# Performance work log

Measured on AMD Instinct MI355X. Metric: run time of the kernel, lower is better.

The kernel has to match this reference:

```python
import jax, jax.numpy as jnp
import numpy as np

# NF4 codebook (from bitsandbytes/torchao)
NF4 = jnp.array([
    -1.0, -0.6961928009986877, -0.5250730514526367, -0.39491748809814453,
    -0.28444138169288635, -0.18477343022823334, -0.09105003625154495, 0.0,
    0.07958029955625534, 0.16093020141124725, 0.24611230194568634,
    0.33791524171829224, 0.44070982933044434, 0.5626170039176941,
    0.7229568362236023, 1.0], dtype=jnp.float32)

IN_DIM, OUT_DIM = 4096, 4096
RANK, ALPHA = 16, 32.0
BLOCK = 64            # nf4 quantization block size
SCALER_BLOCK = 256    # double-quantization block size for scalers


def setup_inputs() -> dict:
    key = jax.random.key(0)
    kx, kw, ka, kb = jax.random.split(key, 4)
    x = jax.random.normal(kx, (4, 2048, IN_DIM), jnp.float32)
    # float base weight, then quantize to NF4 with double-quantized scalers
    w = jax.random.normal(kw, (OUT_DIM, IN_DIM), jnp.float32) * 0.02
    blocks = w.reshape(-1, BLOCK)                          # [n_blocks, 64]
    scalers = jnp.max(jnp.abs(blocks), axis=1)             # per-block absmax
    scaler_mean = jnp.mean(scalers, keepdims=True)         # [1]
    sc = (scalers - scaler_mean).reshape(-1, SCALER_BLOCK) # [n_sblocks, 256]
    q_factor = 127.0 / jnp.max(jnp.abs(sc), axis=1)        # [n_sblocks]
    q_scalers = jnp.clip(jnp.round(sc * q_factor[:, None]), -127, 127)
    q_scalers = q_scalers.astype(jnp.int32).reshape(-1)    # [n_blocks]
    # map normalized values to nearest NF4 code via bucket midpoints
    norm = blocks / scalers[:, None]
    mid = (NF4[:-1] + NF4[1:]) * 0.5
    nf4_idx = jnp.searchsorted(mid, norm).astype(jnp.int32)  # [n_blocks, 64]
    # LoRA weights (kaiming-uniform-like)
    lora_a_w = jax.random.uniform(ka, (RANK, IN_DIM), jnp.float32, -1.0, 1.0) / jnp.sqrt(IN_DIM)
    lora_b_w = jax.random.uniform(kb, (OUT_DIM, RANK), jnp.float32, -1.0, 1.0) / jnp.sqrt(RANK)
    return dict(x=x, nf4_idx=nf4_idx, q_scalers=q_scalers, q_factor=q_factor,
                scaler_mean=scaler_mean, lora_a_w=lora_a_w, lora_b_w=lora_b_w)


def _dequant_nf4(nf4_idx, q_scalers, q_factor, scaler_mean):
    # dequantize double-quantized scalers, then blocks
    scalers = q_scalers.astype(jnp.float32) / jnp.repeat(q_factor, SCALER_BLOCK) + scaler_mean[0]
    w = NF4[nf4_idx] * scalers[:, None]                    # [n_blocks, 64]
    return w.reshape(OUT_DIM, IN_DIM)


def reference(x, nf4_idx, q_scalers, q_factor, scaler_mean, lora_a_w, lora_b_w):
    w = _dequant_nf4(nf4_idx, q_scalers, q_factor, scaler_mean)  # [out, in]
    base = jnp.einsum('bsd,od->bso', x, w)
    # dropout p=0.0 -> identity
    lora = jnp.einsum('bsr,or->bso', jnp.einsum('bsd,rd->bsr', x, lora_a_w), lora_b_w)
    return base + (ALPHA / RANK) * lora
```

## Files before the change

### kernel.cpp

```cpp
#include <hip/hip_runtime.h>
#include <hip/hip_bf16.h>

typedef unsigned short u16;
typedef u16 u16x4 __attribute__((ext_vector_type(4)));
typedef __bf16 bf16x8 __attribute__((ext_vector_type(8)));
typedef float f32x4 __attribute__((ext_vector_type(4)));

#define IN_DIM 4096
#define OUT_DIM 4096
#define M_TOT 8192

__device__ __constant__ float NF4_LUT[16] = {
    -1.0f, -0.6961928009986877f, -0.5250730514526367f, -0.39491748809814453f,
    -0.28444138169288635f, -0.18477343022823334f, -0.09105003625154495f, 0.0f,
    0.07958029955625534f, 0.16093020141124725f, 0.24611230194568634f,
    0.33791524171829224f, 0.44070982933044434f, 0.5626170039176941f,
    0.7229568362236023f, 1.0f};

__device__ __forceinline__ u16 f2bf(float f) {
  unsigned i = __float_as_uint(f);
  i += 0x7fffu + ((i >> 16) & 1u);
  return (u16)(i >> 16);
}

__global__ __launch_bounds__(256) void convert_x(
    const float4* __restrict__ xin, u16x4* __restrict__ xout, int n4)
{
  int i = blockIdx.x * 256 + threadIdx.x;
  const int stride = gridDim.x * 256;
  for (; i < n4; i += stride) {
    const float4 v = xin[i];
    u16x4 o;
    o.x = f2bf(v.x); o.y = f2bf(v.y); o.z = f2bf(v.z); o.w = f2bf(v.w);
    xout[i] = o;
  }
}

__global__ __launch_bounds__(256) void dequant_fold(
    const int* __restrict__ nf4_idx, const int* __restrict__ q_scalers,
    const float* __restrict__ q_factor, const float* __restrict__ scaler_mean,
    const float* __restrict__ lora_a, const float* __restrict__ lora_b,
    u16* __restrict__ w_eff)
{
  __shared__ float s_lut[16];
  __shared__ float s_b[16];
  __shared__ float s_scl[64];
  const int t = threadIdx.x;
  const int o = blockIdx.x;
  if (t < 16) {
    s_lut[t] = NF4_LUT[t];
    s_b[t] = 2.0f * lora_b[o * 16 + t];
  }
  if (t < 64) {
    const int b = o * 64 + t;
    s_scl[t] = (float)q_scalers[b] / q_factor[b >> 8] + scaler_mean[0];
  }
  __syncthreads();

  float Bf[16];
#pragma unroll
  for (int r = 0; r < 16; ++r) Bf[r] = s_b[r];

#pragma unroll
  for (int it = 0; it < 4; ++it) {
    const int d0 = it * 1024 + t * 4;
    const int4 iv = *(const int4*)(nf4_idx + (size_t)o * IN_DIM + d0);
    const float sc = s_scl[d0 >> 6];
    float l0 = 0.f, l1 = 0.f, l2 = 0.f, l3 = 0.f;
#pragma unroll
    for (int r = 0; r < 16; ++r) {
      const float4 av = *(const float4*)(lora_a + (size_t)r * IN_DIM + d0);
      const float br = Bf[r];
      l0 += br * av.x;
      l1 += br * av.y;
      l2 += br * av.z;
      l3 += br * av.w;
    }
    u16x4 ov;
    ov.x = f2bf(s_lut[iv.x] * sc + l0);
    ov.y = f2bf(s_lut[iv.y] * sc + l1);
    ov.z = f2bf(s_lut[iv.z] * sc + l2);
    ov.w = f2bf(s_lut[iv.w] * sc + l3);
    *(u16x4*)(w_eff + (size_t)o * IN_DIM + d0) = ov;
  }
}

#define BM 256
#define BN 256
#define BK 64
#define NT (IN_DIM / BK)

__device__ __forceinline__ void async16(const u16* g, const u16* l) {
  __builtin_amdgcn_global_load_lds(
      (const __attribute__((address_space(1))) void*)g,
      (__attribute__((address_space(3))) void*)l,
      16, 0, 0);
}

#define STG(c, kt, j) do {                                                     \
    async16(gA + (size_t)(j) * 64 * IN_DIM + (kt),                             \
            &sA[(c) * BM * BK + ((j) * 512 + wid * 64) * 8]);                  \
    async16(gB + (size_t)(j) * 64 * IN_DIM + (kt),                             \
            &sB[(c) * BN * BK + ((j) * 512 + wid * 64) * 8]);                  \
  } while (0)

#define MFMA_Q(AF, BF, MI0) do {                                               \
    _Pragma("unroll") for (int mi = (MI0); mi < (MI0) + 4; ++mi)               \
    _Pragma("unroll") for (int ni = 0; ni < 4; ++ni)                           \
      acc[mi][ni] = __builtin_amdgcn_mfma_f32_16x16x32_bf16(                   \
          AF[mi], BF[ni], acc[mi][ni], 0, 0, 0);                               \
  } while (0)

#define KTILE(c, ktn, DOSTAGE, ENDVM_STR, DOENDBAR) do {                       \
                        \
  _Pragma("unroll") for (int mi = 0; mi < 8; ++mi)                             \
    a0[mi] = *(const bf16x8*)&sA[(c) * BM * BK + aBase + mi * 1024 + e0];      \
  _Pragma("unroll") for (int ni = 0; ni < 4; ++ni)                             \
    b0[ni] = *(const bf16x8*)&sB[(c) * BN * BK + bBase + ni * 1024 + e0];      \
  __builtin_amdgcn_s_barrier();                                                \
  asm volatile("s_waitcnt lgkmcnt(0)" ::: "memory");                           \
  __builtin_amdgcn_s_setprio(1);                                               \
  MFMA_Q(a0, b0, 0);                                                           \
  __builtin_amdgcn_s_setprio(0);                                               \
  __builtin_amdgcn_s_barrier();                                                \
                        \
  _Pragma("unroll") for (int mi = 0; mi < 8; ++mi)                             \
    a1[mi] = *(const bf16x8*)&sA[(c) * BM * BK + aBase + mi * 1024 + e1];      \
  _Pragma("unroll") for (int ni = 0; ni < 4; ++ni)                             \
    b1[ni] = *(const bf16x8*)&sB[(c) * BN * BK + bBase + ni * 1024 + e1];      \
  __builtin_amdgcn_s_barrier();                                                \
  asm volatile("s_waitcnt lgkmcnt(0)" ::: "memory");                           \
  __builtin_amdgcn_s_setprio(1);                                               \
  MFMA_Q(a0, b0, 4);                                                           \
  __builtin_amdgcn_s_setprio(0);                                               \
  __builtin_amdgcn_s_barrier();                                                \
                   \
  if (DOSTAGE) { STG(c, ktn, 0); STG(c, ktn, 1); }                             \
  __builtin_amdgcn_s_barrier();                                                \
  __builtin_amdgcn_s_setprio(1);                                               \
  MFMA_Q(a1, b1, 0);                                                           \
  __builtin_amdgcn_s_setprio(0);                                               \
  __builtin_amdgcn_s_barrier();                                                \
                \
  if (DOSTAGE) { STG(c, ktn, 2); STG(c, ktn, 3); }                             \
  __builtin_amdgcn_s_barrier();                                                \
  __builtin_amdgcn_s_setprio(1);                                               \
  MFMA_Q(a1, b1, 4);                                                           \
  __builtin_amdgcn_s_setprio(0);                                               \
  asm volatile("s_waitcnt " ENDVM_STR ::: "memory");                           \
  if (DOENDBAR) __builtin_amdgcn_s_barrier();                                  \
} while (0)

__global__ __launch_bounds__(512, 2) void gemm256(
    const u16* __restrict__ X, const u16* __restrict__ W,
    float* __restrict__ Out)
{
  __shared__ __align__(16) u16 sA[2 * BM * BK];
  __shared__ __align__(16) u16 sB[2 * BN * BK];

  const int tid = threadIdx.x;
  const int lane = tid & 63;
  const int wid = tid >> 6;
  const int wm = wid >> 2;
  const int wn = wid & 3;

  const int bid = blockIdx.x;
  const int swzb = (bid & 7) * 64 + (bid >> 3);
  const int tileM = swzb >> 4;
  const int tileN = swzb & 15;
  const int rowBase = tileM * BM;
  const int colBase = tileN * BN;

  const int cr = tid >> 3;
  const int cq = tid & 7;
  const int qsw = cq ^ (cr & 7);
  const u16* gA = X + (size_t)(rowBase + cr) * IN_DIM + qsw * 8;
  const u16* gB = W + (size_t)(colBase + cr) * IN_DIM + qsw * 8;

  const int l15 = lane & 15;
  const int qhi = lane >> 4;
  const int l7 = lane & 7;
  const int e0 = (qhi ^ l7) * 8;
  const int e1 = ((4 + qhi) ^ l7) * 8;
  const int aBase = (wm * 128 + l15) * 64;
  const int bBase = (wn * 64 + l15) * 64;

  f32x4 acc[8][4] = {};
  bf16x8 a0[8], a1[8], b0[4], b1[4];

  STG(0, 0, 0); STG(0, 0, 1); STG(0, 0, 2); STG(0, 0, 3);
  STG(1, BK, 0); STG(1, BK, 1); STG(1, BK, 2); STG(1, BK, 3);
  asm volatile("s_waitcnt vmcnt(8)" ::: "memory");
  __builtin_amdgcn_s_barrier();

  int kt2 = 2 * BK;
  for (int t = 0; t < NT - 2; t += 2) {
    KTILE(0, kt2, true, "vmcnt(8)", true);
    KTILE(1, kt2 + BK, true, "vmcnt(8)", true);
    kt2 += 2 * BK;
  }
  KTILE(0, 0, false, "vmcnt(0)", true);
  KTILE(1, 0, false, "vmcnt(0)", false);

  const int or4 = qhi * 4;
#pragma unroll
  for (int mi = 0; mi < 8; ++mi) {
#pragma unroll
    for (int i = 0; i < 4; ++i) {
      const size_t r = (size_t)(rowBase + wm * 128 + mi * 16 + or4 + i);
      float* po = Out + r * OUT_DIM + colBase + wn * 64 + l15;
#pragma unroll
      for (int ni = 0; ni < 4; ++ni)
        po[ni * 16] = acc[mi][ni][i];
    }
  }
}

extern "C" void kernel_launch(void* const* d_in, const int* in_sizes, int n_in,
                              void* d_out, int out_size, void* d_ws, size_t ws_size,
                              hipStream_t stream) {
  const float* x         = (const float*)d_in[0];
  const int* nf4_idx     = (const int*)d_in[1];
  const int* q_scalers   = (const int*)d_in[2];
  const float* q_factor  = (const float*)d_in[3];
  const float* scaler_mean = (const float*)d_in[4];
  const float* lora_a    = (const float*)d_in[5];
  const float* lora_b    = (const float*)d_in[6];
  float* out = (float*)d_out;

  const size_t xbf_bytes = (size_t)M_TOT * IN_DIM * sizeof(u16);
  const size_t wef_bytes = (size_t)OUT_DIM * IN_DIM * sizeof(u16);
  if (ws_size < xbf_bytes + wef_bytes) return;
  u16* xbf   = (u16*)d_ws;
  u16* w_eff = (u16*)((char*)d_ws + xbf_bytes);

  hipLaunchKernelGGL(convert_x, dim3(8192), dim3(256), 0, stream,
                     (const float4*)x, (u16x4*)xbf, M_TOT * IN_DIM / 4);
  hipLaunchKernelGGL(dequant_fold, dim3(OUT_DIM), dim3(256), 0, stream,
                     nf4_idx, q_scalers, q_factor, scaler_mean, lora_a, lora_b,
                     w_eff);
  hipLaunchKernelGGL(gemm256, dim3((M_TOT / BM) * (OUT_DIM / BN)), dim3(512),
                     0, stream, xbf, w_eff, out);
}
```

Baseline: 569.1 us.

## Restructure GEMM k-tile into quadrant MFMA phases with split cross-buffer prefetch

Each k-tile now loads A and B fragments for both k-halves in low/high quadrants and issues MFMAs over four output quadrants (LL, HH, LH, HL), reusing loaded fragments across phases. Global-to-LDS staging is interleaved at finer granularity, with half of the next tile's stores issued into the other buffer early and the rest issued into the current buffer after it is consumed. Partial lgkmcnt waits let LDS reads overlap barriers. This aims to hide LDS read latency and smooth memory issue against MFMA work, at the cost of more complex buffer hazard reasoning and different register pressure.

```diff
diff --git a/kernel.cpp b/kernel.cpp
--- a/kernel.cpp
+++ b/kernel.cpp
@@ -104,51 +104,60 @@
             &sB[(c) * BN * BK + ((j) * 512 + wid * 64) * 8]);                  \
   } while (0)
 
-#define MFMA_Q(AF, BF, MI0) do {                                               \
-    _Pragma("unroll") for (int mi = (MI0); mi < (MI0) + 4; ++mi)               \
-    _Pragma("unroll") for (int ni = 0; ni < 4; ++ni)                           \
-      acc[mi][ni] = __builtin_amdgcn_mfma_f32_16x16x32_bf16(                   \
-          AF[mi], BF[ni], acc[mi][ni], 0, 0, 0);                               \
+#define MFMA16(AF, BF, MO, NO) do {                                            \
+    _Pragma("unroll") for (int mi = 0; mi < 4; ++mi)                           \
+    _Pragma("unroll") for (int ni = 0; ni < 2; ++ni)                           \
+    _Pragma("unroll") for (int kr = 0; kr < 2; ++kr)                           \
+      acc[(MO) + mi][(NO) + ni] = __builtin_amdgcn_mfma_f32_16x16x32_bf16(     \
+          AF[mi][kr], BF[ni][kr], acc[(MO) + mi][(NO) + ni], 0, 0, 0);         \
   } while (0)
 
-#define KTILE(c, ktn, DOSTAGE, ENDVM_STR, DOENDBAR) do {                       \
-                        \
-  _Pragma("unroll") for (int mi = 0; mi < 8; ++mi)                             \
-    a0[mi] = *(const bf16x8*)&sA[(c) * BM * BK + aBase + mi * 1024 + e0];      \
-  _Pragma("unroll") for (int ni = 0; ni < 4; ++ni)                             \
-    b0[ni] = *(const bf16x8*)&sB[(c) * BN * BK + bBase + ni * 1024 + e0];      \
+#define KTILE(c, kA, kB, DO01, DO23, DOVM, VMSTR) do {                         \
+                                                                      \
+  _Pragma("unroll") for (int mi = 0; mi < 4; ++mi)                             \
+  _Pragma("unroll") for (int kr = 0; kr < 2; ++kr)                             \
+    aL[mi][kr] = *(const bf16x8*)&sA[(c) * BM * BK + aBase + mi * 1024 + e[kr]];\
+  _Pragma("unroll") for (int ni = 0; ni < 2; ++ni)                             \
+  _Pragma("unroll") for (int kr = 0; kr < 2; ++kr)                             \
+    bL[ni][kr] = *(const bf16x8*)&sB[(c) * BN * BK + bBase + ni * 1024 + e[kr]];\
+  if (DO01) STG(1 - (c), kA, 2);                                               \
+  asm volatile("s_waitcnt lgkmcnt(8)" ::: "memory");                           \
   __builtin_amdgcn_s_barrier();                                                \
   asm volatile("s_waitcnt lgkmcnt(0)" ::: "memory");                           \
   __builtin_amdgcn_s_setprio(1);                                               \
-  MFMA_Q(a0, b0, 0);                                                           \
-  __builtin_amdgcn_s_setprio(0);                                               \
-  __builtin_amdgcn_s_barrier();                                                \
-                        \
-  _Pragma("unroll") for (int mi = 0; mi < 8; ++mi)                             \
-    a1[mi] = *(const bf16x8*)&sA[(c) * BM * BK + aBase + mi * 1024 + e1];      \
-  _Pragma("unroll") for (int ni = 0; ni < 4; ++ni)                             \
-    b1[ni] = *(const bf16x8*)&sB[(c) * BN * BK + bBase + ni * 1024 + e1];      \
+  MFMA16(aL, bL, 0, 0);                                                        \
+  __builtin_amdgcn_s_setprio(0);                                               \
+  __builtin_amdgcn_s_barrier();                                                \
+                                                                      \
+  _Pragma("unroll") for (int mi = 0; mi < 4; ++mi)                             \
+  _Pragma("unroll") for (int kr = 0; kr < 2; ++kr)                             \
+    aH[mi][kr] = *(const bf16x8*)&sA[(c) * BM * BK + aBase + 4096 + mi * 1024 + e[kr]];\
+  _Pragma("unroll") for (int ni = 0; ni < 2; ++ni)                             \
+  _Pragma("unroll") for (int kr = 0; kr < 2; ++kr)                             \
+    bH[ni][kr] = *(const bf16x8*)&sB[(c) * BN * BK + bBase + 2048 + ni * 1024 + e[kr]];\
+  if (DO01) STG(1 - (c), kA, 3);                                               \
+  asm volatile("s_waitcnt lgkmcnt(8)" ::: "memory");                           \
   __builtin_amdgcn_s_barrier();                                                \
   asm volatile("s_waitcnt lgkmcnt(0)" ::: "memory");                           \
   __builtin_amdgcn_s_setprio(1);                                               \
-  MFMA_Q(a0, b0, 4);                                                           \
-  __builtin_amdgcn_s_setprio(0);                                               \
-  __builtin_amdgcn_s_barrier();                                                \
-                   \
-  if (DOSTAGE) { STG(c, ktn, 0); STG(c, ktn, 1); }                             \
-  __builtin_amdgcn_s_barrier();                                                \
-  __builtin_amdgcn_s_setprio(1);                                               \
-  MFMA_Q(a1, b1, 0);                                                           \
+  MFMA16(aH, bH, 4, 2);                                                        \
   __builtin_amdgcn_s_setprio(0);                                               \
   __builtin_amdgcn_s_barrier();                                                \
                 \
-  if (DOSTAGE) { STG(c, ktn, 2); STG(c, ktn, 3); }                             \
-  __builtin_amdgcn_s_barrier();                                                \
-  __builtin_amdgcn_s_setprio(1);                                               \
-  MFMA_Q(a1, b1, 4);                                                           \
-  __builtin_amdgcn_s_setprio(0);                                               \
-  asm volatile("s_waitcnt " ENDVM_STR ::: "memory");                           \
-  if (DOENDBAR) __builtin_amdgcn_s_barrier();                                  \
+  if (DO23) STG(c, kB, 0);                                                     \
+  __builtin_amdgcn_s_barrier();                                                \
+  __builtin_amdgcn_s_setprio(1);                                               \
+  MFMA16(aL, bH, 0, 2);                                                        \
+  __builtin_amdgcn_s_setprio(0);                                               \
+  __builtin_amdgcn_s_barrier();                                                \
+                                                                      \
+  if (DO23) STG(c, kB, 1);                                                     \
+  __builtin_amdgcn_s_barrier();                                                \
+  __builtin_amdgcn_s_setprio(1);                                               \
+  MFMA16(aH, bL, 4, 0);                                                        \
+  __builtin_amdgcn_s_setprio(0);                                               \
+  if (DOVM) { asm volatile("s_waitcnt " VMSTR ::: "memory"); }                  \
+  __builtin_amdgcn_s_barrier();                                                \
 } while (0)
 
 __global__ __launch_bounds__(512, 2) void gemm256(
@@ -180,27 +189,28 @@
   const int l15 = lane & 15;
   const int qhi = lane >> 4;
   const int l7 = lane & 7;
-  const int e0 = (qhi ^ l7) * 8;
-  const int e1 = ((4 + qhi) ^ l7) * 8;
+  int e[2];
+  e[0] = (qhi ^ l7) * 8;
+  e[1] = ((4 + qhi) ^ l7) * 8;
   const int aBase = (wm * 128 + l15) * 64;
   const int bBase = (wn * 64 + l15) * 64;
 
   f32x4 acc[8][4] = {};
-  bf16x8 a0[8], a1[8], b0[4], b1[4];
+  bf16x8 aL[4][2], aH[4][2], bL[2][2], bH[2][2];
 
   STG(0, 0, 0); STG(0, 0, 1); STG(0, 0, 2); STG(0, 0, 3);
-  STG(1, BK, 0); STG(1, BK, 1); STG(1, BK, 2); STG(1, BK, 3);
-  asm volatile("s_waitcnt vmcnt(8)" ::: "memory");
+  STG(1, BK, 0); STG(1, BK, 1);
+  asm volatile("s_waitcnt vmcnt(4)" ::: "memory");
   __builtin_amdgcn_s_barrier();
 
-  int kt2 = 2 * BK;
+  int kt = 0;
   for (int t = 0; t < NT - 2; t += 2) {
-    KTILE(0, kt2, true, "vmcnt(8)", true);
-    KTILE(1, kt2 + BK, true, "vmcnt(8)", true);
-    kt2 += 2 * BK;
-  }
-  KTILE(0, 0, false, "vmcnt(0)", true);
-  KTILE(1, 0, false, "vmcnt(0)", false);
+    KTILE(0, kt + BK,     kt + 2 * BK, true, true, true, "vmcnt(4)");
+    KTILE(1, kt + 2 * BK, kt + 3 * BK, true, true, true, "vmcnt(4)");
+    kt += 2 * BK;
+  }
+  KTILE(0, (NT - 1) * BK, 0, true, false, true, "vmcnt(0)");
+  KTILE(1, 0, 0, false, false, false, "vmcnt(0)");
 
   const int or4 = qhi * 4;
 #pragma unroll
```

New measurement: 610.1 us. 7.2% more time.
